# Kernel optimization log

Hardware: AMD Instinct MI355X
Metric: run time of the kernel (lower is better)

## Reference

```python
import jax, jax.numpy as jnp
import numpy as np

B, N, D, H = 2, 160, 4096, 4
DH = D // H            # dim_head = 1024
SCALE = DH ** -0.5     # applied twice, as in the torch module


def setup_inputs() -> dict:
    key = jax.random.key(0)
    k1, k2, k3, k4 = jax.random.split(key, 4)
    w_std = 0.02
    return {
        "x": jax.random.normal(k1, (B, N, D), jnp.float32),
        "y": jax.random.normal(k2, (B, N, D), jnp.float32),
        "Wq": jax.random.normal(k3, (D, D), jnp.float32) * w_std,  # to_Q weight (out,in)
        "Wk": jax.random.normal(k4, (D, D), jnp.float32) * w_std,  # to_K weight (out,in)
    }


def reference(x, y, Wq, Wk):
    # q = to_Q(y): (B, N, D); torch Linear computes y @ W^T
    q = y @ Wq.T
    # k = to_K(x) split into heads: (B, H, N, DH)
    k = (x @ Wk.T).reshape(B, N, H, DH).transpose(0, 2, 1, 3)
    # kkt[b,h,i,j] = sum_d k[b,h,i,d] * k[b,h,j,d], scaled -> (B, H, N, N)
    kkt = jnp.einsum('bhid,bhjd->bhij', k, k) * SCALE
    # q is replicated across heads in the original (repeat), so contract
    # directly with the head-free q: dots[b,h,i,j] = sum_m q[b,m,i] * kkt[b,h,j,m]
    # -> (B, H, D, N), scaled again
    dots = jnp.einsum('bmi,bhjm->bhij', q, kkt) * SCALE
    attn = jax.nn.softplus(dots)
    # flatten(1) then reshape(40, 32, D): row-major, so a single reshape
    return attn.reshape(40, 32, D)
```

## Files before the change

### kernel.cpp

```cpp
#include <hip/hip_runtime.h>
#include <hip/hip_bf16.h>


typedef __attribute__((ext_vector_type(4))) float  f32x4;
typedef __attribute__((ext_vector_type(8))) __bf16 bf16x8;
typedef __attribute__((ext_vector_type(4))) __bf16 bf16x4;

#define SCALE 0.03125f

static __device__ __forceinline__ f32x4 mfma16(bf16x8 a, bf16x8 b, f32x4 c) {
    return __builtin_amdgcn_mfma_f32_16x16x32_bf16(a, b, c, 0, 0, 0);
}

static __device__ __forceinline__ bf16x8 pack8(float4 a, float4 b) {
    bf16x8 r;
    r[0] = (__bf16)a.x; r[1] = (__bf16)a.y; r[2] = (__bf16)a.z; r[3] = (__bf16)a.w;
    r[4] = (__bf16)b.x; r[5] = (__bf16)b.y; r[6] = (__bf16)b.z; r[7] = (__bf16)b.w;
    return r;
}

static __device__ __forceinline__ bf16x8 pack8f(const float* v) {
    bf16x8 r;
    #pragma unroll
    for (int i = 0; i < 8; ++i) r[i] = (__bf16)v[i];
    return r;
}

static __device__ __forceinline__ float softplus(float x) {
    return fmaxf(x, 0.0f) + log1pf(expf(-fabsf(x)));
}

static __device__ __forceinline__ void gload_lds16(const void* g, void* l) {
    __builtin_amdgcn_global_load_lds((const __attribute__((address_space(1))) void*)g,
                                     (__attribute__((address_space(3))) void*)l,
                                     16, 0, 0);
}

__global__ __launch_bounds__(256)
void cvt_kernel(const float* __restrict__ x, const float* __restrict__ y,
                __bf16* __restrict__ xb, __bf16* __restrict__ yb)
{
    const float* src = blockIdx.y ? y : x;
    __bf16* dst = blockIdx.y ? yb : xb;
    size_t i = ((size_t)blockIdx.x * 256 + threadIdx.x) * 8;
    float4 a = *(const float4*)(src + i);
    float4 b = *(const float4*)(src + i + 4);
    *(bf16x8*)(dst + i) = pack8(a, b);
}

__global__ __launch_bounds__(256)
void qk_gemm(const __bf16* __restrict__ yb, const __bf16* __restrict__ xb,
             const float* __restrict__ Wq, const float* __restrict__ Wk,
             float* __restrict__ P)
{
    const int z  = blockIdx.y;
    const int ks = blockIdx.z;
    const __bf16* __restrict__ Ab = z ? xb : yb;
    const float*  __restrict__ W  = z ? Wk : Wq;
    const int bn = blockIdx.x * 32;
    const int kb = ks * 2048;

    __shared__ __bf16 lA[2][320 * 32];
    __shared__ __bf16 lB[2][32 * 32];

    const int tid  = threadIdx.x;
    const int lane = tid & 63;
    const int wid  = tid >> 6;

    const int ar    = tid >> 2;
    const int aslot = (tid & 3) ^ ((tid >> 3) & 3);
    const __bf16* ag = Ab + (size_t)ar * 4096 + kb + aslot * 8;

    const int wrow  = tid >> 3;
    const int chunk = tid & 7;
    const int bdst  = wrow * 32 + (((chunk >> 1) ^ ((wrow >> 1) & 3)) << 3)
                    + ((chunk & 1) << 2);
    const float* wg = W + (size_t)(bn + wrow) * 4096 + kb + chunk * 4;

    f32x4 acc[5][2] = {};

    {
        #pragma unroll
        for (int i = 0; i < 5; ++i)
            gload_lds16(ag + (size_t)i * 64 * 4096,
                        (char*)&lA[0][0] + i * 4096 + wid * 1024);
        float4 w = *(const float4*)wg;
        bf16x4 bv; bv[0]=(__bf16)w.x; bv[1]=(__bf16)w.y; bv[2]=(__bf16)w.z; bv[3]=(__bf16)w.w;
        *(bf16x4*)&lB[0][bdst] = bv;
    }
    __syncthreads();

    int cur = 0;
    for (int s = 0; s < 64; ++s) {
        float4 wnext;
        if (s < 63) {
            const __bf16* agn = ag + (s + 1) * 32;
            #pragma unroll
            for (int i = 0; i < 5; ++i)
                gload_lds16(agn + (size_t)i * 64 * 4096,
                            (char*)&lA[cur ^ 1][0] + i * 4096 + wid * 1024);
            wnext = *(const float4*)(wg + (s + 1) * 32);
        }

        const int c = lane >> 4;
        bf16x8 bfr[2];
        #pragma unroll
        for (int jn = 0; jn < 2; ++jn) {
            const int j = jn * 16 + (lane & 15);
            bfr[jn] = *(const bf16x8*)&lB[cur][j * 32 + ((c ^ ((j >> 1) & 3)) << 3)];
        }
        #pragma unroll
        for (int m = 0; m < 5; ++m) {
            const int row = wid * 80 + m * 16 + (lane & 15);
            bf16x8 afr = *(const bf16x8*)&lA[cur][row * 32 + ((c ^ ((row >> 1) & 3)) << 3)];
            acc[m][0] = mfma16(afr, bfr[0], acc[m][0]);
            acc[m][1] = mfma16(afr, bfr[1], acc[m][1]);
        }

        if (s < 63) {
            bf16x4 bv; bv[0]=(__bf16)wnext.x; bv[1]=(__bf16)wnext.y;
                      bv[2]=(__bf16)wnext.z; bv[3]=(__bf16)wnext.w;
            *(bf16x4*)&lB[cur ^ 1][bdst] = bv;
        }
        __syncthreads();
        cur ^= 1;
    }

    float* Pz = P + ((size_t)(z * 2 + ks)) * 320 * 4096;
    #pragma unroll
    for (int m = 0; m < 5; ++m) {
        const int row0 = wid * 80 + m * 16 + ((lane >> 4) << 2);
        #pragma unroll
        for (int jn = 0; jn < 2; ++jn) {
            const int col = bn + jn * 16 + (lane & 15);
            #pragma unroll
            for (int r = 0; r < 4; ++r)
                Pz[(size_t)(row0 + r) * 4096 + col] = acc[m][jn][r];
        }
    }
}

__global__ __launch_bounds__(256)
void reduce_kernel(const float* __restrict__ P,
                   __bf16* __restrict__ qT, __bf16* __restrict__ kout)
{
    const int z    = blockIdx.z;
    const int col0 = blockIdx.x * 64;
    const int row0 = blockIdx.y * 64;
    const float* P0 = P + ((size_t)z * 2 + 0) * 320 * 4096;
    const float* P1 = P + ((size_t)z * 2 + 1) * 320 * 4096;

    const int t  = threadIdx.x;
    const int r  = t >> 2;
    const int cc = (t & 3) * 16;

    float v[16];
    {
        size_t base = (size_t)(row0 + r) * 4096 + col0 + cc;
        #pragma unroll
        for (int i = 0; i < 4; ++i) {
            float4 a = *(const float4*)(P0 + base + i * 4);
            float4 b = *(const float4*)(P1 + base + i * 4);
            v[i*4+0] = a.x + b.x; v[i*4+1] = a.y + b.y;
            v[i*4+2] = a.z + b.z; v[i*4+3] = a.w + b.w;
        }
    }

    if (z == 1) {
        __bf16* dst = kout + (size_t)(row0 + r) * 4096 + col0 + cc;
        *(bf16x8*)dst       = pack8f(v);
        *(bf16x8*)(dst + 8) = pack8f(v + 8);
        return;
    }

    __shared__ float lt[64][65];
    #pragma unroll
    for (int i = 0; i < 16; ++i) lt[r][cc + i] = v[i];
    __syncthreads();

    const int col = t & 63;
    const int rr0 = (t >> 6) * 16;
    float w[16];
    #pragma unroll
    for (int i = 0; i < 16; ++i) w[i] = lt[rr0 + i][col];

    const int gr = row0 + rr0;
    const int b  = gr >= 160;
    const int ri = gr - b * 160;
    __bf16* dst = qT + (size_t)b * 4096 * 160 + (size_t)(col0 + col) * 160 + ri;
    *(bf16x8*)dst       = pack8f(w);
    *(bf16x8*)(dst + 8) = pack8f(w + 8);
}

__global__ __launch_bounds__(64)
void kkt_kernel(const __bf16* __restrict__ kmat, __bf16* __restrict__ kkt)
{
    const int bh = blockIdx.x;
    const int b  = bh >> 2, h = bh & 3;
    const int i0 = blockIdx.y * 16;
    const int j0 = blockIdx.z * 16;
    const int lane = threadIdx.x;

    const __bf16* base = kmat + (size_t)b * 160 * 4096 + h * 1024;
    const int ko = (lane >> 4) << 3;
    const __bf16* pa = base + (size_t)(i0 + (lane & 15)) * 4096 + ko;
    const __bf16* pb = base + (size_t)(j0 + (lane & 15)) * 4096 + ko;

    f32x4 acc = {};
    #pragma unroll 4
    for (int kk = 0; kk < 1024; kk += 32) {
        bf16x8 a  = *(const bf16x8*)(pa + kk);
        bf16x8 bb = *(const bf16x8*)(pb + kk);
        acc = mfma16(a, bb, acc);
    }

    #pragma unroll
    for (int r = 0; r < 4; ++r) {
        int i = i0 + ((lane >> 4) << 2) + r;
        int j = j0 + (lane & 15);
        kkt[((size_t)bh * 160 + i) * 160 + j] = (__bf16)(acc[r] * SCALE);
    }
}

__global__ __launch_bounds__(256)
void dots_kernel(const __bf16* __restrict__ qT, const __bf16* __restrict__ kkt,
                 float* __restrict__ out)
{
    const int bh   = blockIdx.z;
    const int b    = bh >> 2;
    const int lane = threadIdx.x & 63;
    const int wid  = threadIdx.x >> 6;
    const int i0   = blockIdx.x * 64 + wid * 16;
    const int j0   = blockIdx.y * 32;

    const __bf16* Ab = qT + (size_t)b * 4096 * 160;
    const __bf16* Bb = kkt + (size_t)bh * 160 * 160;
    const int ko = (lane >> 4) << 3;
    const __bf16* pa  = Ab + (size_t)(i0 + (lane & 15)) * 160 + ko;
    const __bf16* pb0 = Bb + (size_t)(j0 + (lane & 15)) * 160 + ko;
    const __bf16* pb1 = pb0 + 16 * 160;

    f32x4 acc0 = {}, acc1 = {};
    #pragma unroll
    for (int m0 = 0; m0 < 160; m0 += 32) {
        bf16x8 a  = *(const bf16x8*)(pa + m0);
        bf16x8 b0 = *(const bf16x8*)(pb0 + m0);
        bf16x8 b1 = *(const bf16x8*)(pb1 + m0);
        acc0 = mfma16(a, b0, acc0);
        acc1 = mfma16(a, b1, acc1);
    }

    #pragma unroll
    for (int r = 0; r < 4; ++r) {
        int i = i0 + ((lane >> 4) << 2) + r;
        int j = j0 + (lane & 15);
        size_t o = ((size_t)bh * 4096 + i) * 160 + j;
        out[o]      = softplus(acc0[r] * SCALE);
        out[o + 16] = softplus(acc1[r] * SCALE);
    }
}

extern "C" void kernel_launch(void* const* d_in, const int* in_sizes, int n_in,
                              void* d_out, int out_size, void* d_ws, size_t ws_size,
                              hipStream_t stream)
{
    const float* x  = (const float*)d_in[0];
    const float* y  = (const float*)d_in[1];
    const float* Wq = (const float*)d_in[2];
    const float* Wk = (const float*)d_in[3];
    float* out = (float*)d_out;

    __bf16* qT  = (__bf16*)d_ws;
    __bf16* kbf = qT  + (size_t)2 * 4096 * 160;
    __bf16* kkt = kbf + (size_t)320 * 4096;
    __bf16* xb  = kkt + (size_t)8 * 160 * 160;
    __bf16* yb  = xb  + (size_t)320 * 4096;
    float*  P   = (float*)(yb + (size_t)320 * 4096);
    P = (float*)(((uintptr_t)P + 15) & ~(uintptr_t)15);

    cvt_kernel   <<<dim3(640, 2),    256, 0, stream>>>(x, y, xb, yb);
    qk_gemm      <<<dim3(128, 2, 2), 256, 0, stream>>>(yb, xb, Wq, Wk, P);
    reduce_kernel<<<dim3(64, 5, 2),  256, 0, stream>>>(P, qT, kbf);
    kkt_kernel   <<<dim3(8, 10, 10),  64, 0, stream>>>(kbf, kkt);
    dots_kernel  <<<dim3(64, 5, 8),  256, 0, stream>>>(qT, kkt, out);
}
```

Baseline: 106.3 us.

## Triple-buffer A tiles in qk_gemm with explicit waitcnt and prefetch distance two

Reworks the qk_gemm main loop to use three LDS buffers for the activation tile and prefetch two K-steps ahead. Fine-grained s_waitcnt vmcnt counts plus raw s_barrier replace __syncthreads, so loads stay in flight across the barrier. All fragments are read from LDS before the MFMAs, which run at raised wave priority via s_setprio. This adds LDS usage and relies on hand-counted vmcnt values, so a miscount could cause races.

Result: faster. 100.3 us (-5.6%).

```diff
diff --git a/kernel.cpp b/kernel.cpp
--- a/kernel.cpp
+++ b/kernel.cpp
@@ -60,8 +60,8 @@
     const int bn = blockIdx.x * 32;
     const int kb = ks * 2048;
 
-    __shared__ __bf16 lA[2][320 * 32];
-    __shared__ __bf16 lB[2][32 * 32];
+    __shared__ __bf16 lA[3 * 320 * 32];
+    __shared__ __bf16 lB[2 * 32 * 32];
 
     const int tid  = threadIdx.x;
     const int lane = tid & 63;
@@ -73,57 +73,82 @@
 
     const int wrow  = tid >> 3;
     const int chunk = tid & 7;
-    const int bdst  = wrow * 32 + (((chunk >> 1) ^ ((wrow >> 1) & 3)) << 3)
-                    + ((chunk & 1) << 2);
+    const int bofs  = wrow * 64 + (((chunk >> 1) ^ ((wrow >> 1) & 3)) << 4)
+                    + ((chunk & 1) << 3);
     const float* wg = W + (size_t)(bn + wrow) * 4096 + kb + chunk * 4;
 
+    char* LA = (char*)lA;
+    char* LB = (char*)lB;
+
     f32x4 acc[5][2] = {};
 
+    #pragma unroll
+    for (int i = 0; i < 5; ++i)
+        gload_lds16(ag + (size_t)i * 64 * 4096, LA + i * 4096 + wid * 1024);
+    float4 w0 = *(const float4*)wg;
+    #pragma unroll
+    for (int i = 0; i < 5; ++i)
+        gload_lds16(ag + 32 + (size_t)i * 64 * 4096, LA + 20480 + i * 4096 + wid * 1024);
+    float4 w1 = *(const float4*)(wg + 32);
+
+    asm volatile("s_waitcnt vmcnt(6)" ::: "memory");
     {
-        #pragma unroll
-        for (int i = 0; i < 5; ++i)
-            gload_lds16(ag + (size_t)i * 64 * 4096,
-                        (char*)&lA[0][0] + i * 4096 + wid * 1024);
-        float4 w = *(const float4*)wg;
-        bf16x4 bv; bv[0]=(__bf16)w.x; bv[1]=(__bf16)w.y; bv[2]=(__bf16)w.z; bv[3]=(__bf16)w.w;
-        *(bf16x4*)&lB[0][bdst] = bv;
-    }
-    __syncthreads();
-
-    int cur = 0;
+        bf16x4 bv; bv[0]=(__bf16)w0.x; bv[1]=(__bf16)w0.y;
+                   bv[2]=(__bf16)w0.z; bv[3]=(__bf16)w0.w;
+        *(bf16x4*)(LB + bofs) = bv;
+    }
+    asm volatile("s_waitcnt lgkmcnt(0)" ::: "memory");
+    __builtin_amdgcn_s_barrier();
+
+    int a_cur = 0, a_nxt = 20480, a_nx2 = 40960;
+    int b_cur = 0, b_nxt = 2048;
+    float4 wcur = w1;
+
+    const int c4 = (lane >> 4) << 4;
+
     for (int s = 0; s < 64; ++s) {
-        float4 wnext;
-        if (s < 63) {
-            const __bf16* agn = ag + (s + 1) * 32;
+        bf16x8 bfr[2];
+        #pragma unroll
+        for (int jn = 0; jn < 2; ++jn) {
+            int j = jn * 16 + (lane & 15);
+            bfr[jn] = *(const bf16x8*)(LB + b_cur + j * 64 + (c4 ^ (((j >> 1) & 3) << 4)));
+        }
+        bf16x8 afr[5];
+        #pragma unroll
+        for (int m = 0; m < 5; ++m) {
+            int row = wid * 80 + m * 16 + (lane & 15);
+            afr[m] = *(const bf16x8*)(LA + a_cur + row * 64 + (c4 ^ (((row >> 1) & 3) << 4)));
+        }
+
+        float4 wnew = wcur;
+        if (s < 62) {
+            const __bf16* agp = ag + (s + 2) * 32;
             #pragma unroll
             for (int i = 0; i < 5; ++i)
-                gload_lds16(agn + (size_t)i * 64 * 4096,
-                            (char*)&lA[cur ^ 1][0] + i * 4096 + wid * 1024);
-            wnext = *(const float4*)(wg + (s + 1) * 32);
-        }
-
-        const int c = lane >> 4;
-        bf16x8 bfr[2];
-        #pragma unroll
-        for (int jn = 0; jn < 2; ++jn) {
-            const int j = jn * 16 + (lane & 15);
-            bfr[jn] = *(const bf16x8*)&lB[cur][j * 32 + ((c ^ ((j >> 1) & 3)) << 3)];
-        }
+                gload_lds16(agp + (size_t)i * 64 * 4096, LA + a_nx2 + i * 4096 + wid * 1024);
+            wnew = *(const float4*)(wg + (s + 2) * 32);
+        }
+
+        __builtin_amdgcn_s_setprio(1);
         #pragma unroll
         for (int m = 0; m < 5; ++m) {
-            const int row = wid * 80 + m * 16 + (lane & 15);
-            bf16x8 afr = *(const bf16x8*)&lA[cur][row * 32 + ((c ^ ((row >> 1) & 3)) << 3)];
-            acc[m][0] = mfma16(afr, bfr[0], acc[m][0]);
-            acc[m][1] = mfma16(afr, bfr[1], acc[m][1]);
-        }
+            acc[m][0] = mfma16(afr[m], bfr[0], acc[m][0]);
+            acc[m][1] = mfma16(afr[m], bfr[1], acc[m][1]);
+        }
+        __builtin_amdgcn_s_setprio(0);
 
         if (s < 63) {
-            bf16x4 bv; bv[0]=(__bf16)wnext.x; bv[1]=(__bf16)wnext.y;
-                      bv[2]=(__bf16)wnext.z; bv[3]=(__bf16)wnext.w;
-            *(bf16x4*)&lB[cur ^ 1][bdst] = bv;
-        }
-        __syncthreads();
-        cur ^= 1;
+            bf16x4 bv; bv[0]=(__bf16)wcur.x; bv[1]=(__bf16)wcur.y;
+                       bv[2]=(__bf16)wcur.z; bv[3]=(__bf16)wcur.w;
+            *(bf16x4*)(LB + b_nxt + bofs) = bv;
+            if (s < 62) asm volatile("s_waitcnt vmcnt(6) lgkmcnt(0)" ::: "memory");
+            else        asm volatile("s_waitcnt vmcnt(0) lgkmcnt(0)" ::: "memory");
+            __builtin_amdgcn_s_barrier();
+        }
+
+        int t = a_cur; a_cur = a_nxt; a_nxt = a_nx2; a_nx2 = t;
+        t = b_cur; b_cur = b_nxt; b_nxt = t;
+        wcur = wnew;
     }
 
     float* Pz = P + ((size_t)(z * 2 + ks)) * 320 * 4096;
```

## Retile projection GEMM to 64-wide N with 4-way split-K and bf16 partials

Applied to the files above, without the earlier changes.

The projection GEMM is restructured. Each block now computes a 320x64 tile over a quarter of K, with 64-deep K steps, register-staged loads in place of global_load_lds, XOR-swizzled LDS and raised MFMA priority. Partial sums are written as bf16 instead of fp32 and reduced over four slices, which cuts partial-sum traffic but loses some precision. Nontemporal loads and stores are added in the convert, GEMM and output kernels. The grid is remapped to 512 blocks with a launch bound targeting two blocks per CU.

Result: slower. 112.5 us (+5.8%).

```diff
diff --git a/kernel.cpp b/kernel.cpp
--- a/kernel.cpp
+++ b/kernel.cpp
@@ -4,7 +4,6 @@
 
 typedef __attribute__((ext_vector_type(4))) float  f32x4;
 typedef __attribute__((ext_vector_type(8))) __bf16 bf16x8;
-typedef __attribute__((ext_vector_type(4))) __bf16 bf16x4;
 
 #define SCALE 0.03125f
 
@@ -12,10 +11,10 @@
     return __builtin_amdgcn_mfma_f32_16x16x32_bf16(a, b, c, 0, 0, 0);
 }
 
-static __device__ __forceinline__ bf16x8 pack8(float4 a, float4 b) {
+static __device__ __forceinline__ bf16x8 pack8(f32x4 a, f32x4 b) {
     bf16x8 r;
-    r[0] = (__bf16)a.x; r[1] = (__bf16)a.y; r[2] = (__bf16)a.z; r[3] = (__bf16)a.w;
-    r[4] = (__bf16)b.x; r[5] = (__bf16)b.y; r[6] = (__bf16)b.z; r[7] = (__bf16)b.w;
+    #pragma unroll
+    for (int i = 0; i < 4; ++i) { r[i] = (__bf16)a[i]; r[4 + i] = (__bf16)b[i]; }
     return r;
 }
 
@@ -28,12 +27,6 @@
 
 static __device__ __forceinline__ float softplus(float x) {
     return fmaxf(x, 0.0f) + log1pf(expf(-fabsf(x)));
-}
-
-static __device__ __forceinline__ void gload_lds16(const void* g, void* l) {
-    __builtin_amdgcn_global_load_lds((const __attribute__((address_space(1))) void*)g,
-                                     (__attribute__((address_space(3))) void*)l,
-                                     16, 0, 0);
 }
 
 __global__ __launch_bounds__(256)
@@ -43,112 +36,124 @@
     const float* src = blockIdx.y ? y : x;
     __bf16* dst = blockIdx.y ? yb : xb;
     size_t i = ((size_t)blockIdx.x * 256 + threadIdx.x) * 8;
-    float4 a = *(const float4*)(src + i);
-    float4 b = *(const float4*)(src + i + 4);
+    f32x4 a = __builtin_nontemporal_load((const f32x4*)(src + i));
+    f32x4 b = __builtin_nontemporal_load((const f32x4*)(src + i + 4));
     *(bf16x8*)(dst + i) = pack8(a, b);
 }
 
-__global__ __launch_bounds__(256)
+__global__ __launch_bounds__(256, 2)
 void qk_gemm(const __bf16* __restrict__ yb, const __bf16* __restrict__ xb,
              const float* __restrict__ Wq, const float* __restrict__ Wk,
-             float* __restrict__ P)
-{
-    const int z  = blockIdx.y;
-    const int ks = blockIdx.z;
-    const __bf16* __restrict__ Ab = z ? xb : yb;
-    const float*  __restrict__ W  = z ? Wk : Wq;
-    const int bn = blockIdx.x * 32;
-    const int kb = ks * 2048;
-
-    __shared__ __bf16 lA[2][320 * 32];
-    __shared__ __bf16 lB[2][32 * 32];
+             __bf16* __restrict__ P)
+{
+    const int key = blockIdx.x & 7;
+    const int z   = key >> 2;
+    const int ks  = key & 3;
+    const int np  = blockIdx.x >> 3;
+    const int bn  = np * 64;
+    const int kc  = ks * 1024;
+
+    __shared__ __bf16 lA[320 * 64];
+    __shared__ __bf16 lW[64 * 64];
 
     const int tid  = threadIdx.x;
     const int lane = tid & 63;
     const int wid  = tid >> 6;
-
-    const int ar    = tid >> 2;
-    const int aslot = (tid & 3) ^ ((tid >> 3) & 3);
-    const __bf16* ag = Ab + (size_t)ar * 4096 + kb + aslot * 8;
-
-    const int wrow  = tid >> 3;
-    const int chunk = tid & 7;
-    const int bdst  = wrow * 32 + (((chunk >> 1) ^ ((wrow >> 1) & 3)) << 3)
-                    + ((chunk & 1) << 2);
-    const float* wg = W + (size_t)(bn + wrow) * 4096 + kb + chunk * 4;
-
-    f32x4 acc[5][2] = {};
-
-    {
-        #pragma unroll
-        for (int i = 0; i < 5; ++i)
-            gload_lds16(ag + (size_t)i * 64 * 4096,
-                        (char*)&lA[0][0] + i * 4096 + wid * 1024);
-        float4 w = *(const float4*)wg;
-        bf16x4 bv; bv[0]=(__bf16)w.x; bv[1]=(__bf16)w.y; bv[2]=(__bf16)w.z; bv[3]=(__bf16)w.w;
-        *(bf16x4*)&lB[0][bdst] = bv;
-    }
-    __syncthreads();
-
-    int cur = 0;
-    for (int s = 0; s < 64; ++s) {
-        float4 wnext;
-        if (s < 63) {
-            const __bf16* agn = ag + (s + 1) * 32;
-            #pragma unroll
-            for (int i = 0; i < 5; ++i)
-                gload_lds16(agn + (size_t)i * 64 * 4096,
-                            (char*)&lA[cur ^ 1][0] + i * 4096 + wid * 1024);
-            wnext = *(const float4*)(wg + (s + 1) * 32);
-        }
-
-        const int c = lane >> 4;
-        bf16x8 bfr[2];
-        #pragma unroll
-        for (int jn = 0; jn < 2; ++jn) {
-            const int j = jn * 16 + (lane & 15);
-            bfr[jn] = *(const bf16x8*)&lB[cur][j * 32 + ((c ^ ((j >> 1) & 3)) << 3)];
-        }
-        #pragma unroll
-        for (int m = 0; m < 5; ++m) {
-            const int row = wid * 80 + m * 16 + (lane & 15);
-            bf16x8 afr = *(const bf16x8*)&lA[cur][row * 32 + ((c ^ ((row >> 1) & 3)) << 3)];
-            acc[m][0] = mfma16(afr, bfr[0], acc[m][0]);
-            acc[m][1] = mfma16(afr, bfr[1], acc[m][1]);
-        }
-
-        if (s < 63) {
-            bf16x4 bv; bv[0]=(__bf16)wnext.x; bv[1]=(__bf16)wnext.y;
-                      bv[2]=(__bf16)wnext.z; bv[3]=(__bf16)wnext.w;
-            *(bf16x4*)&lB[cur ^ 1][bdst] = bv;
-        }
+    const int li   = lane & 15;
+    const int lk   = lane >> 4;
+
+    const __bf16* __restrict__ Ab = z ? xb : yb;
+    const float*  __restrict__ Wm = z ? Wk : Wq;
+
+    const int arow  = tid >> 3;
+    const int aslot = tid & 7;
+    const int aswz  = (aslot ^ (arow & 7)) * 8;
+    const __bf16* ag = Ab + (size_t)arow * 4096 + kc + aslot * 8;
+
+    const int wrow = tid >> 2;
+    const float* wg = Wm + (size_t)(bn + wrow) * 4096 + kc + (tid & 3) * 16;
+    const int wsl0 = ((((tid & 3) << 1))     ^ (wrow & 7)) * 8;
+    const int wsl1 = ((((tid & 3) << 1) | 1) ^ (wrow & 7)) * 8;
+
+    f32x4 acc[5][4] = {};
+    bf16x8 areg[10];
+    f32x4  wreg[4];
+
+    #pragma unroll
+    for (int p = 0; p < 10; ++p)
+        areg[p] = *(const bf16x8*)(ag + (size_t)p * 32 * 4096);
+    #pragma unroll
+    for (int i = 0; i < 4; ++i)
+        wreg[i] = __builtin_nontemporal_load((const f32x4*)(wg + i * 4));
+
+    for (int s = 0; s < 16; ++s) {
         __syncthreads();
-        cur ^= 1;
-    }
-
-    float* Pz = P + ((size_t)(z * 2 + ks)) * 320 * 4096;
+        #pragma unroll
+        for (int p = 0; p < 10; ++p)
+            *(bf16x8*)&lA[(p * 32 + arow) * 64 + aswz] = areg[p];
+        *(bf16x8*)&lW[wrow * 64 + wsl0] = pack8(wreg[0], wreg[1]);
+        *(bf16x8*)&lW[wrow * 64 + wsl1] = pack8(wreg[2], wreg[3]);
+        __syncthreads();
+
+        if (s < 15) {
+            #pragma unroll
+            for (int p = 0; p < 10; ++p)
+                areg[p] = *(const bf16x8*)(ag + (size_t)p * 32 * 4096 + (s + 1) * 64);
+            #pragma unroll
+            for (int i = 0; i < 4; ++i)
+                wreg[i] = __builtin_nontemporal_load((const f32x4*)(wg + (s + 1) * 64 + i * 4));
+        }
+
+        #pragma unroll
+        for (int kk = 0; kk < 2; ++kk) {
+            const int slot = kk * 4 + lk;
+            bf16x8 wf[4], af[5];
+            #pragma unroll
+            for (int jn = 0; jn < 4; ++jn) {
+                const int j = jn * 16 + li;
+                wf[jn] = *(const bf16x8*)&lW[j * 64 + ((slot ^ (j & 7)) << 3)];
+            }
+            #pragma unroll
+            for (int m = 0; m < 5; ++m) {
+                const int rr = wid * 80 + m * 16 + li;
+                af[m] = *(const bf16x8*)&lA[rr * 64 + ((slot ^ (rr & 7)) << 3)];
+            }
+            __builtin_amdgcn_s_setprio(1);
+            #pragma unroll
+            for (int m = 0; m < 5; ++m)
+                #pragma unroll
+                for (int jn = 0; jn < 4; ++jn)
+                    acc[m][jn] = mfma16(af[m], wf[jn], acc[m][jn]);
+            __builtin_amdgcn_s_setprio(0);
+        }
+    }
+
+    __bf16* Pz = P + (size_t)key * 320 * 4096;
     #pragma unroll
     for (int m = 0; m < 5; ++m) {
-        const int row0 = wid * 80 + m * 16 + ((lane >> 4) << 2);
-        #pragma unroll
-        for (int jn = 0; jn < 2; ++jn) {
-            const int col = bn + jn * 16 + (lane & 15);
+        const int row0 = wid * 80 + m * 16 + lk * 4;
+        #pragma unroll
+        for (int jn = 0; jn < 4; ++jn) {
+            const int col = bn + jn * 16 + li;
             #pragma unroll
             for (int r = 0; r < 4; ++r)
-                Pz[(size_t)(row0 + r) * 4096 + col] = acc[m][jn][r];
+                __builtin_nontemporal_store((__bf16)acc[m][jn][r],
+                                            &Pz[(size_t)(row0 + r) * 4096 + col]);
         }
     }
 }
 
 __global__ __launch_bounds__(256)
-void reduce_kernel(const float* __restrict__ P,
+void reduce_kernel(const __bf16* __restrict__ P,
                    __bf16* __restrict__ qT, __bf16* __restrict__ kout)
 {
     const int z    = blockIdx.z;
     const int col0 = blockIdx.x * 64;
     const int row0 = blockIdx.y * 64;
-    const float* P0 = P + ((size_t)z * 2 + 0) * 320 * 4096;
-    const float* P1 = P + ((size_t)z * 2 + 1) * 320 * 4096;
+    const __bf16* P0 = P + ((size_t)z * 4 + 0) * 320 * 4096;
+    const __bf16* P1 = P + ((size_t)z * 4 + 1) * 320 * 4096;
+    const __bf16* P2 = P + ((size_t)z * 4 + 2) * 320 * 4096;
+    const __bf16* P3 = P + ((size_t)z * 4 + 3) * 320 * 4096;
 
     const int t  = threadIdx.x;
     const int r  = t >> 2;
@@ -158,11 +163,14 @@
     {
         size_t base = (size_t)(row0 + r) * 4096 + col0 + cc;
         #pragma unroll
-        for (int i = 0; i < 4; ++i) {
-            float4 a = *(const float4*)(P0 + base + i * 4);
-            float4 b = *(const float4*)(P1 + base + i * 4);
-            v[i*4+0] = a.x + b.x; v[i*4+1] = a.y + b.y;
-            v[i*4+2] = a.z + b.z; v[i*4+3] = a.w + b.w;
+        for (int i = 0; i < 2; ++i) {
+            bf16x8 a = *(const bf16x8*)(P0 + base + i * 8);
+            bf16x8 b = *(const bf16x8*)(P1 + base + i * 8);
+            bf16x8 c = *(const bf16x8*)(P2 + base + i * 8);
+            bf16x8 d = *(const bf16x8*)(P3 + base + i * 8);
+            #pragma unroll
+            for (int j = 0; j < 8; ++j)
+                v[i * 8 + j] = (float)a[j] + (float)b[j] + (float)c[j] + (float)d[j];
         }
     }
 
@@ -255,8 +263,8 @@
         int i = i0 + ((lane >> 4) << 2) + r;
         int j = j0 + (lane & 15);
         size_t o = ((size_t)bh * 4096 + i) * 160 + j;
-        out[o]      = softplus(acc0[r] * SCALE);
-        out[o + 16] = softplus(acc1[r] * SCALE);
+        __builtin_nontemporal_store(softplus(acc0[r] * SCALE), &out[o]);
+        __builtin_nontemporal_store(softplus(acc1[r] * SCALE), &out[o + 16]);
     }
 }
 
@@ -275,11 +283,10 @@
     __bf16* kkt = kbf + (size_t)320 * 4096;
     __bf16* xb  = kkt + (size_t)8 * 160 * 160;
     __bf16* yb  = xb  + (size_t)320 * 4096;
-    float*  P   = (float*)(yb + (size_t)320 * 4096);
-    P = (float*)(((uintptr_t)P + 15) & ~(uintptr_t)15);
+    __bf16* P   = yb  + (size_t)320 * 4096;
 
     cvt_kernel   <<<dim3(640, 2),    256, 0, stream>>>(x, y, xb, yb);
-    qk_gemm      <<<dim3(128, 2, 2), 256, 0, stream>>>(yb, xb, Wq, Wk, P);
+    qk_gemm      <<<dim3(512),       256, 0, stream>>>(yb, xb, Wq, Wk, P);
     reduce_kernel<<<dim3(64, 5, 2),  256, 0, stream>>>(P, qT, kbf);
     kkt_kernel   <<<dim3(8, 10, 10),  64, 0, stream>>>(kbf, kkt);
     dots_kernel  <<<dim3(64, 5, 8),  256, 0, stream>>>(qT, kkt, out);
```
